# Kernel tuning notes

Measured on AMD Instinct MI355X. Metric: run time of the kernel, lower is better.

## Reference

```python
import jax, jax.numpy as jnp
import numpy as np

EPS = 1e-5      # BatchNorm1d eps
THETA = 1.0     # spike threshold
ALPHA = 5.0     # ATan surrogate alpha

@jax.custom_vjp
def atan_spike(x):
    # forward: heaviside; backward: ATan surrogate gradient
    return (x > 0).astype(x.dtype)

def _spike_fwd(x):
    return atan_spike(x), x

def _spike_bwd(x, g):
    return (g * ALPHA / (2.0 * (1.0 + (jnp.pi / 2.0 * ALPHA * x) ** 2)),)

atan_spike.defvjp(_spike_fwd, _spike_bwd)

def _lif_layer(x, W, beta_raw, gamma, bias, readout):
    # x: [T,B,J], W: [I,J]
    x = jnp.einsum('tbj,ij->tbi', x, W)
    # BatchNorm1d over (T*B) samples, per channel (training-mode batch stats)
    mean = jnp.mean(x, axis=(0, 1))
    var = jnp.var(x, axis=(0, 1))
    x = (x - mean) * jax.lax.rsqrt(var + EPS) * gamma + bias
    beta = jax.nn.sigmoid(beta_raw)
    B, I = x.shape[1], x.shape[2]
    U0 = jnp.zeros((B, I), x.dtype)
    if readout:
        def step(Ut, xt):
            Ut = beta * Ut + (1.0 - beta) * xt
            return Ut, Ut
        _, o = jax.lax.scan(step, U0, x)
    else:
        def step(carry, xt):
            Ut, St = carry
            Ut = beta * (Ut - THETA * St) + (1.0 - beta) * xt
            St = atan_spike(Ut - THETA)
            return (Ut, St), St
        _, o = jax.lax.scan(step, (U0, U0), x)
    return o  # [T,B,I]

def setup_inputs():
    key = jax.random.key(0)
    ks = jax.random.split(key, 8)
    B, T, J, H, O = 128, 512, 700, 512, 20
    def kaiming(k, out_dim, in_dim):
        # kaiming_uniform_(a=sqrt(5)) -> bound = 1/sqrt(fan_in)
        bound = 1.0 / np.sqrt(in_dim)
        return jax.random.uniform(k, (out_dim, in_dim), jnp.float32, -bound, bound)
    return {
        'x': jax.random.normal(ks[0], (B, T, J), jnp.float32),
        'W1': kaiming(ks[1], H, J),
        'beta1': jax.random.uniform(ks[2], (H,), jnp.float32, 0.0, 1.0),
        'g1': jnp.ones((H,), jnp.float32),
        'b1': jnp.zeros((H,), jnp.float32),
        'W2': kaiming(ks[3], H, H),
        'beta2': jax.random.uniform(ks[4], (H,), jnp.float32, 0.0, 1.0),
        'g2': jnp.ones((H,), jnp.float32),
        'b2': jnp.zeros((H,), jnp.float32),
        'Wr': kaiming(ks[5], O, H),
        'betar': jax.random.uniform(ks[6], (O,), jnp.float32, 0.0, 1.0),
        'gr': jnp.ones((O,), jnp.float32),
        'br': jnp.zeros((O,), jnp.float32),
    }

def reference(x, W1, beta1, g1, b1, W2, beta2, g2, b2, Wr, betar, gr, br):
    h = jnp.transpose(x, (1, 0, 2))  # [B,T,J] -> [T,B,J]
    h = _lif_layer(h, W1, beta1, g1, b1, readout=False)
    h = _lif_layer(h, W2, beta2, g2, b2, readout=False)
    h = _lif_layer(h, Wr, betar, gr, br, readout=True)
    p = jax.nn.softmax(h, axis=2)  # [T,B,O]
    return p.sum(axis=0)           # [B,O]
```

## Files before the change

kernel.cpp:

```cpp
#include <hip/hip_runtime.h>
#include <math.h>

typedef _Float16 f16_t;
typedef _Float16 f16x2 __attribute__((ext_vector_type(2)));
typedef _Float16 f16x8 __attribute__((ext_vector_type(8)));
typedef float f32x4 __attribute__((ext_vector_type(4)));

constexpr int Bn = 128;
constexpr int Tn = 512;
constexpr int Jn = 700;
constexpr int Jp = 704;
constexpr int Hn = 512;
constexpr int On = 20;
constexpr int Mn = Bn * Tn;

#define LDS_U32(p) ((__attribute__((address_space(3))) uint32_t*)(p))
#define GLB_U32(p) ((const __attribute__((address_space(1))) uint32_t*)(p))

template <int NT, bool SWZ>
__global__ __launch_bounds__(512, 4) void gemm_f16(
    const f16_t* __restrict__ A, const f16_t* __restrict__ W,
    float* __restrict__ C, float* __restrict__ s_out, float* __restrict__ q_out,
    int LDA, int LDW, int pairs, int Nout)
{
    constexpr int JT = 2 * NT;
    __shared__ __align__(16) f16_t sA[2 * 4096];
    __shared__ __align__(16) f16_t sW[2 * NT * 4096];

    int bx, by;
    if (SWZ) {
        const int g = blockIdx.x;
        by = (g >> 4) * 8 + (g & 7);
        bx = (g >> 3) & 1;
    } else {
        bx = blockIdx.x;
        by = blockIdx.y;
    }
    const int tid  = threadIdx.x;
    const int bm   = by * 128;
    const int bn   = bx * (NT * 128);
    const int lane = tid & 63;
    const int wv   = tid >> 6;
    const int wm   = (wv & 1) * 64;
    const int wn   = (wv >> 1) * (NT * 32);
    const int fr   = lane & 15;
    const int quad = lane >> 4;
    const int srow = lane >> 2;
    const int scol = (((lane & 3) ^ ((lane >> 3) & 3)) * 8);
    const int ksw  = ((quad ^ ((fr >> 1) & 3)) * 8);

    f32x4 acc[4][JT];
#pragma unroll
    for (int i = 0; i < 4; ++i)
#pragma unroll
        for (int j = 0; j < JT; ++j) acc[i][j] = {0.f, 0.f, 0.f, 0.f};

    for (int p = 0; p < pairs; ++p) {
#pragma unroll
        for (int cc = 0; cc < 2; ++cc) {
            const int c  = wv + cc * 8;
            const int s  = c >> 3;
            const int cr = (c & 7) * 16;
            const int kA = p * 64 + s * 32;
            const uint32_t off = __builtin_amdgcn_readfirstlane(s * 8192 + cr * 64);
            const f16_t* gp = A + (size_t)(bm + cr + srow) * LDA + kA + scol;
            __builtin_amdgcn_global_load_lds(GLB_U32(gp), LDS_U32((char*)sA + off), 16, 0, 0);
        }
#pragma unroll
        for (int cc = 0; cc < 2 * NT; ++cc) {
            const int c   = wv + cc * 8;
            const int h   = c / (NT * 8);
            const int rem = c % (NT * 8);
            const int nt  = rem >> 3;
            const int cr  = (rem & 7) * 16;
            const int kW  = p * 64 + h * 32;
            const uint32_t off = __builtin_amdgcn_readfirstlane((h * NT + nt) * 8192 + cr * 64);
            const f16_t* gp = W + (size_t)(bn + nt * 128 + cr + srow) * LDW + kW + scol;
            __builtin_amdgcn_global_load_lds(GLB_U32(gp), LDS_U32((char*)sW + off), 16, 0, 0);
        }
        __syncthreads();

#pragma unroll
        for (int h = 0; h < 2; ++h) {
            f16x8 av[4];
#pragma unroll
            for (int i = 0; i < 4; ++i)
                av[i] = *(const f16x8*)&sA[h * 4096 + (wm + i * 16 + fr) * 32 + ksw];
            f16x8 wf[JT];
#pragma unroll
            for (int jt = 0; jt < JT; ++jt) {
                const int n = wn + jt * 16 + fr;
                wf[jt] = *(const f16x8*)&sW[(h * NT + (n >> 7)) * 4096 + (n & 127) * 32 + ksw];
            }
#pragma unroll
            for (int i = 0; i < 4; ++i)
#pragma unroll
                for (int jt = 0; jt < JT; ++jt)
                    acc[i][jt] = __builtin_amdgcn_mfma_f32_16x16x32_f16(av[i], wf[jt], acc[i][jt], 0, 0, 0);
        }
        __syncthreads();
    }

#pragma unroll
    for (int jt = 0; jt < JT; ++jt) {
        const int gcol = bn + wn + jt * 16 + fr;
        float s = 0.f, q = 0.f;
        if (gcol < Nout) {
#pragma unroll
            for (int i = 0; i < 4; ++i) {
#pragma unroll
                for (int rg = 0; rg < 4; ++rg) {
                    const float v = acc[i][jt][rg];
                    C[(size_t)(bm + wm + i * 16 + quad * 4 + rg) * Nout + gcol] = v;
                    s += v;
                    q += v * v;
                }
            }
        }
        s += __shfl_xor(s, 16); s += __shfl_xor(s, 32);
        q += __shfl_xor(q, 16); q += __shfl_xor(q, 32);
        if (quad == 0 && gcol < Nout) {
            atomicAdd(&s_out[gcol], s);
            atomicAdd(&q_out[gcol], q);
        }
    }
}

__global__ __launch_bounds__(256) void conv_x(const float* __restrict__ x,
                                              f16_t* __restrict__ A1) {
    const int idx = blockIdx.x * 256 + threadIdx.x;
    const int m = idx / 88, g = idx % 88;
    const int k8 = g * 8;
    const float* rp = x + (size_t)m * Jn + k8;
    float f[8];
    if (k8 + 8 <= Jn) {
        const float4 v0 = *(const float4*)rp;
        const float4 v1 = *(const float4*)(rp + 4);
        f[0] = v0.x; f[1] = v0.y; f[2] = v0.z; f[3] = v0.w;
        f[4] = v1.x; f[5] = v1.y; f[6] = v1.z; f[7] = v1.w;
    } else {
#pragma unroll
        for (int e = 0; e < 8; ++e) f[e] = (k8 + e < Jn) ? rp[e] : 0.f;
    }
    f16x8 hv;
#pragma unroll
    for (int e = 0; e < 8; ++e) hv[e] = (f16_t)f[e];
    *(f16x8*)&A1[(size_t)m * Jp + k8] = hv;
}

__global__ __launch_bounds__(256) void conv_w(const float* __restrict__ Wsrc,
                                              f16_t* __restrict__ Wo,
                                              int N, int K, int KP, int NP) {
    const int idx = blockIdx.x * 256 + threadIdx.x;
    if (idx >= NP * (KP / 8)) return;
    const int n = idx / (KP / 8), g = idx % (KP / 8);
    const int k8 = g * 8;
    f16x8 hv;
#pragma unroll
    for (int e = 0; e < 8; ++e) {
        const float f = (n < N && k8 + e < K) ? Wsrc[(size_t)n * K + k8 + e] : 0.f;
        hv[e] = (f16_t)f;
    }
    *(f16x8*)&Wo[(size_t)n * KP + k8] = hv;
}

__global__ __launch_bounds__(256) void lif_scan(const float* __restrict__ X,
                                                f16_t* __restrict__ S_out,
                                                const float* __restrict__ sums,
                                                const float* __restrict__ sumsq,
                                                const float* __restrict__ beta_raw,
                                                const float* __restrict__ gamma,
                                                const float* __restrict__ bias) {
    const int gid = blockIdx.x * 256 + threadIdx.x;
    const int b  = gid >> 8;
    const int cq = gid & 255;
    const int i0 = cq * 2;

    float g[2], bi[2], bt[2], ob[2];
#pragma unroll
    for (int e = 0; e < 2; ++e) {
        const int i = i0 + e;
        const float invM = 1.f / (float)Mn;
        const float mean = sums[i] * invM;
        const float var  = sumsq[i] * invM - mean * mean;
        const float inv  = rsqrtf(var + 1e-5f);
        g[e]  = gamma[i] * inv;
        bi[e] = bias[i] - mean * g[e];
        bt[e] = 1.f / (1.f + expf(-beta_raw[i]));
        ob[e] = 1.f - bt[e];
    }

    const float2* Xp = (const float2*)(X + (size_t)b * Tn * Hn) + cq;
    f16x2* Sp2 = (f16x2*)(S_out + (size_t)b * Tn * Hn) + cq;

    float U[2] = {0.f, 0.f}, Sp[2] = {0.f, 0.f};
#pragma unroll 8
    for (int t = 0; t < Tn; ++t) {
        const float2 v = Xp[(size_t)t * (Hn / 2)];
        const float vf[2] = {v.x, v.y};
        f16x2 so;
#pragma unroll
        for (int e = 0; e < 2; ++e) {
            const float xt = vf[e] * g[e] + bi[e];
            U[e] = bt[e] * (U[e] - Sp[e]) + ob[e] * xt;
            Sp[e] = (U[e] > 1.0f) ? 1.0f : 0.0f;
            so[e] = (f16_t)Sp[e];
        }
        Sp2[(size_t)t * (Hn / 2)] = so;
    }
}

__global__ __launch_bounds__(256) void readout_kernel(const float* __restrict__ A,
                                                      const float* __restrict__ sums,
                                                      const float* __restrict__ sumsq,
                                                      const float* __restrict__ beta_raw,
                                                      const float* __restrict__ gamma,
                                                      const float* __restrict__ bias,
                                                      float* __restrict__ out) {
    __shared__ float xs[Tn * On];
    __shared__ float gsh[On], bsh[On], betash[On];
    __shared__ float red[4][On];

    const int b = blockIdx.x;
    const int tid = threadIdx.x;

    if (tid < On) {
        const float invM = 1.f / (float)Mn;
        const float mean = sums[tid] * invM;
        const float var = sumsq[tid] * invM - mean * mean;
        const float inv = rsqrtf(var + 1e-5f);
        const float g = gamma[tid] * inv;
        gsh[tid] = g;
        bsh[tid] = bias[tid] - mean * g;
        betash[tid] = 1.f / (1.f + expf(-beta_raw[tid]));
    }
    __syncthreads();

    const float* Ab = A + (size_t)b * Tn * On;
    for (int idx = tid; idx < Tn * On; idx += 256) {
        const int o = idx % On;
        xs[idx] = Ab[idx] * gsh[o] + bsh[o];
    }
    __syncthreads();

    if (tid < On) {
        const float beta = betash[tid], omb = 1.f - beta;
        float U = 0.f;
        for (int t = 0; t < Tn; ++t) {
            U = beta * U + omb * xs[t * On + tid];
            xs[t * On + tid] = U;
        }
    }
    __syncthreads();

    float part[On];
#pragma unroll
    for (int o = 0; o < On; ++o) part[o] = 0.f;

    for (int t = tid; t < Tn; t += 256) {
        float v[On];
        float m = -1e30f;
#pragma unroll
        for (int o = 0; o < On; ++o) {
            v[o] = xs[t * On + o];
            m = fmaxf(m, v[o]);
        }
        float s = 0.f;
#pragma unroll
        for (int o = 0; o < On; ++o) {
            v[o] = expf(v[o] - m);
            s += v[o];
        }
        const float rs = 1.f / s;
#pragma unroll
        for (int o = 0; o < On; ++o) part[o] += v[o] * rs;
    }

#pragma unroll
    for (int o = 0; o < On; ++o) {
#pragma unroll
        for (int off = 32; off > 0; off >>= 1) part[o] += __shfl_down(part[o], off);
    }
    const int lane = tid & 63, wid = tid >> 6;
    if (lane == 0) {
#pragma unroll
        for (int o = 0; o < On; ++o) red[wid][o] = part[o];
    }
    __syncthreads();
    if (tid < On) out[b * On + tid] = red[0][tid] + red[1][tid] + red[2][tid] + red[3][tid];
}

extern "C" void kernel_launch(void* const* d_in, const int* in_sizes, int n_in,
                              void* d_out, int out_size, void* d_ws, size_t ws_size,
                              hipStream_t stream) {
    const float* x   = (const float*)d_in[0];
    const float* W1  = (const float*)d_in[1];
    const float* be1 = (const float*)d_in[2];
    const float* g1  = (const float*)d_in[3];
    const float* b1  = (const float*)d_in[4];
    const float* W2  = (const float*)d_in[5];
    const float* be2 = (const float*)d_in[6];
    const float* b2g = (const float*)d_in[7];
    const float* b2  = (const float*)d_in[8];
    const float* Wr  = (const float*)d_in[9];
    const float* ber = (const float*)d_in[10];
    const float* gr  = (const float*)d_in[11];
    const float* br  = (const float*)d_in[12];
    float* out = (float*)d_out;

    char* ws = (char*)d_ws;
    const size_t r0Bytes   = (size_t)Mn * Jp * sizeof(f16_t);
    const size_t bufCBytes = (size_t)Mn * Hn * sizeof(float);
    f16_t* A1   = (f16_t*)ws;
    f16_t* bufS = (f16_t*)ws;
    float* bufC = (float*)(ws + r0Bytes);
    char*  p    = ws + r0Bytes + bufCBytes;
    float* bufR = (float*)p;              p += (size_t)Mn * On * sizeof(float);
    f16_t* W1h  = (f16_t*)p;              p += (size_t)Hn * Jp * sizeof(f16_t);
    f16_t* W2h  = (f16_t*)p;              p += (size_t)Hn * Hn * sizeof(f16_t);
    f16_t* Wrh  = (f16_t*)p;              p += (size_t)128 * Hn * sizeof(f16_t);
    float* stats = (float*)p;
    float* s1 = stats;       float* q1 = s1 + Hn;
    float* s2 = q1 + Hn;     float* q2 = s2 + Hn;
    float* s3 = q2 + Hn;     float* q3 = s3 + 32;

    hipMemsetAsync(stats, 0, (4 * Hn + 64) * sizeof(float), stream);

    conv_x<<<(Mn * 88) / 256, 256, 0, stream>>>(x, A1);
    conv_w<<<(Hn * 88 + 255) / 256, 256, 0, stream>>>(W1, W1h, Hn, Jn, Jp, Hn);
    conv_w<<<(Hn * 64 + 255) / 256, 256, 0, stream>>>(W2, W2h, Hn, Hn, Hn, Hn);
    conv_w<<<(128 * 64 + 255) / 256, 256, 0, stream>>>(Wr, Wrh, On, Hn, Hn, 128);

    gemm_f16<2, true><<<2 * (Mn / 128), 512, 0, stream>>>(A1, W1h, bufC, s1, q1,
        Jp, Jp, Jp / 64, Hn);
    lif_scan<<<(Bn * Hn / 2) / 256, 256, 0, stream>>>(bufC, bufS, s1, q1, be1, g1, b1);

    gemm_f16<2, true><<<2 * (Mn / 128), 512, 0, stream>>>(bufS, W2h, bufC, s2, q2,
        Hn, Hn, Hn / 64, Hn);
    lif_scan<<<(Bn * Hn / 2) / 256, 256, 0, stream>>>(bufC, bufS, s2, q2, be2, b2g, b2);

    gemm_f16<1, false><<<dim3(1, Mn / 128), 512, 0, stream>>>(bufS, Wrh, bufR, s3, q3,
        Hn, Hn, Hn / 64, On);
    readout_kernel<<<Bn, 256, 0, stream>>>(bufR, s3, q3, ber, gr, br, out);
}
```

Before: 561.8 us.

## Double-buffer LDS tiles in f16 GEMM to overlap global loads with MFMA

Doubles the LDS staging buffers for the A and W tiles and prefetches the next K-pair into the alternate buffer while the current one is consumed by MFMAs. Explicit vmcnt waits and raw barriers replace __syncthreads. Launch-bound minimum occupancy is now a template parameter, lowered to 2 for the large GEMMs. The extra LDS footprint lowers the possible number of resident workgroups per CU, trading occupancy for latency hiding.

```diff
diff --git a/kernel.cpp b/kernel.cpp
--- a/kernel.cpp
+++ b/kernel.cpp
@@ -17,15 +17,15 @@
 #define LDS_U32(p) ((__attribute__((address_space(3))) uint32_t*)(p))
 #define GLB_U32(p) ((const __attribute__((address_space(1))) uint32_t*)(p))
 
-template <int NT, bool SWZ>
-__global__ __launch_bounds__(512, 4) void gemm_f16(
+template <int NT, bool SWZ, int MINW>
+__global__ __launch_bounds__(512, MINW) void gemm_f16(
     const f16_t* __restrict__ A, const f16_t* __restrict__ W,
     float* __restrict__ C, float* __restrict__ s_out, float* __restrict__ q_out,
     int LDA, int LDW, int pairs, int Nout)
 {
     constexpr int JT = 2 * NT;
-    __shared__ __align__(16) f16_t sA[2 * 4096];
-    __shared__ __align__(16) f16_t sW[2 * NT * 4096];
+    __shared__ __align__(16) f16_t sA[2 * 2 * 4096];
+    __shared__ __align__(16) f16_t sW[2 * 2 * NT * 4096];
 
     int bx, by;
     if (SWZ) {
@@ -55,14 +55,15 @@
 #pragma unroll
         for (int j = 0; j < JT; ++j) acc[i][j] = {0.f, 0.f, 0.f, 0.f};
 
-    for (int p = 0; p < pairs; ++p) {
+    auto stage = [&](int buf, int p) {
 #pragma unroll
         for (int cc = 0; cc < 2; ++cc) {
             const int c  = wv + cc * 8;
             const int s  = c >> 3;
             const int cr = (c & 7) * 16;
             const int kA = p * 64 + s * 32;
-            const uint32_t off = __builtin_amdgcn_readfirstlane(s * 8192 + cr * 64);
+            const uint32_t off =
+                __builtin_amdgcn_readfirstlane(buf * 16384 + s * 8192 + cr * 64);
             const f16_t* gp = A + (size_t)(bm + cr + srow) * LDA + kA + scol;
             __builtin_amdgcn_global_load_lds(GLB_U32(gp), LDS_U32((char*)sA + off), 16, 0, 0);
         }
@@ -74,23 +75,38 @@
             const int nt  = rem >> 3;
             const int cr  = (rem & 7) * 16;
             const int kW  = p * 64 + h * 32;
-            const uint32_t off = __builtin_amdgcn_readfirstlane((h * NT + nt) * 8192 + cr * 64);
+            const uint32_t off = __builtin_amdgcn_readfirstlane(
+                buf * (NT * 16384) + (h * NT + nt) * 8192 + cr * 64);
             const f16_t* gp = W + (size_t)(bn + nt * 128 + cr + srow) * LDW + kW + scol;
             __builtin_amdgcn_global_load_lds(GLB_U32(gp), LDS_U32((char*)sW + off), 16, 0, 0);
         }
-        __syncthreads();
-
+    };
+
+    stage(0, 0);
+    int cur = 0;
+    for (int p = 0; p < pairs; ++p) {
+        if (p + 1 < pairs) {
+            stage(cur ^ 1, p + 1);
+            asm volatile("s_waitcnt vmcnt(%0)" :: "i"(2 + 2 * NT) : "memory");
+        } else {
+            asm volatile("s_waitcnt vmcnt(0)" ::: "memory");
+        }
+        __builtin_amdgcn_s_barrier();
+        __builtin_amdgcn_sched_barrier(0);
+
+        const int aBase = cur * 8192;
+        const int wBase = cur * (NT * 8192);
 #pragma unroll
         for (int h = 0; h < 2; ++h) {
             f16x8 av[4];
 #pragma unroll
             for (int i = 0; i < 4; ++i)
-                av[i] = *(const f16x8*)&sA[h * 4096 + (wm + i * 16 + fr) * 32 + ksw];
+                av[i] = *(const f16x8*)&sA[aBase + h * 4096 + (wm + i * 16 + fr) * 32 + ksw];
             f16x8 wf[JT];
 #pragma unroll
             for (int jt = 0; jt < JT; ++jt) {
                 const int n = wn + jt * 16 + fr;
-                wf[jt] = *(const f16x8*)&sW[(h * NT + (n >> 7)) * 4096 + (n & 127) * 32 + ksw];
+                wf[jt] = *(const f16x8*)&sW[wBase + (h * NT + (n >> 7)) * 4096 + (n & 127) * 32 + ksw];
             }
 #pragma unroll
             for (int i = 0; i < 4; ++i)
@@ -98,7 +114,11 @@
                 for (int jt = 0; jt < JT; ++jt)
                     acc[i][jt] = __builtin_amdgcn_mfma_f32_16x16x32_f16(av[i], wf[jt], acc[i][jt], 0, 0, 0);
         }
-        __syncthreads();
+
+        asm volatile("s_waitcnt lgkmcnt(0)" ::: "memory");
+        __builtin_amdgcn_s_barrier();
+        __builtin_amdgcn_sched_barrier(0);
+        cur ^= 1;
     }
 
 #pragma unroll
@@ -331,15 +351,15 @@
     conv_w<<<(Hn * 64 + 255) / 256, 256, 0, stream>>>(W2, W2h, Hn, Hn, Hn, Hn);
     conv_w<<<(128 * 64 + 255) / 256, 256, 0, stream>>>(Wr, Wrh, On, Hn, Hn, 128);
 
-    gemm_f16<2, true><<<2 * (Mn / 128), 512, 0, stream>>>(A1, W1h, bufC, s1, q1,
+    gemm_f16<2, true, 2><<<2 * (Mn / 128), 512, 0, stream>>>(A1, W1h, bufC, s1, q1,
         Jp, Jp, Jp / 64, Hn);
     lif_scan<<<(Bn * Hn / 2) / 256, 256, 0, stream>>>(bufC, bufS, s1, q1, be1, g1, b1);
 
-    gemm_f16<2, true><<<2 * (Mn / 128), 512, 0, stream>>>(bufS, W2h, bufC, s2, q2,
+    gemm_f16<2, true, 2><<<2 * (Mn / 128), 512, 0, stream>>>(bufS, W2h, bufC, s2, q2,
         Hn, Hn, Hn / 64, Hn);
     lif_scan<<<(Bn * Hn / 2) / 256, 256, 0, stream>>>(bufC, bufS, s2, q2, be2, b2g, b2);
 
-    gemm_f16<1, false><<<dim3(1, Mn / 128), 512, 0, stream>>>(bufS, Wrh, bufR, s3, q3,
+    gemm_f16<1, false, 4><<<dim3(1, Mn / 128), 512, 0, stream>>>(bufS, Wrh, bufR, s3, q3,
         Hn, Hn, Hn / 64, On);
     readout_kernel<<<Bn, 256, 0, stream>>>(bufR, s3, q3, ber, gr, br, out);
 }
```

Result: slower. 593.4 us (+5.6%).

## Fuse fp32-to-fp16 input conversion into first GEMM's A-tile load

Applied to the files above, without the earlier changes.

Removes the separate conv_x kernel, which read the fp32 input and wrote a padded fp16 copy. The first GEMM now loads fp32 x directly into registers, converts it to fp16 and stores it into the swizzled LDS tile, with zero padding at the K tail. This drops a full write and re-read of the large fp16 activation buffer and one kernel launch. In exchange, the A path uses synchronous register loads instead of asynchronous global-to-LDS loads, and fp32 reads are repeated across the two column-block workgroups.

```diff
diff --git a/kernel.cpp b/kernel.cpp
--- a/kernel.cpp
+++ b/kernel.cpp
@@ -17,9 +17,10 @@
 #define LDS_U32(p) ((__attribute__((address_space(3))) uint32_t*)(p))
 #define GLB_U32(p) ((const __attribute__((address_space(1))) uint32_t*)(p))
 
-template <int NT, bool SWZ>
+template <int NT, bool SWZ, bool FUSEA>
 __global__ __launch_bounds__(512, 4) void gemm_f16(
-    const f16_t* __restrict__ A, const f16_t* __restrict__ W,
+    const f16_t* __restrict__ A, const float* __restrict__ Xf,
+    const f16_t* __restrict__ W,
     float* __restrict__ C, float* __restrict__ s_out, float* __restrict__ q_out,
     int LDA, int LDW, int pairs, int Nout)
 {
@@ -49,6 +50,10 @@
     const int scol = (((lane & 3) ^ ((lane >> 3) & 3)) * 8);
     const int ksw  = ((quad ^ ((fr >> 1) & 3)) * 8);
 
+    const int fs  = tid >> 8;
+    const int frw = (tid >> 1) & 127;
+    const int fh  = tid & 1;
+
     f32x4 acc[4][JT];
 #pragma unroll
     for (int i = 0; i < 4; ++i)
@@ -56,15 +61,33 @@
         for (int j = 0; j < JT; ++j) acc[i][j] = {0.f, 0.f, 0.f, 0.f};
 
     for (int p = 0; p < pairs; ++p) {
-#pragma unroll
-        for (int cc = 0; cc < 2; ++cc) {
-            const int c  = wv + cc * 8;
-            const int s  = c >> 3;
-            const int cr = (c & 7) * 16;
-            const int kA = p * 64 + s * 32;
-            const uint32_t off = __builtin_amdgcn_readfirstlane(s * 8192 + cr * 64);
-            const f16_t* gp = A + (size_t)(bm + cr + srow) * LDA + kA + scol;
-            __builtin_amdgcn_global_load_lds(GLB_U32(gp), LDS_U32((char*)sA + off), 16, 0, 0);
+        float fbuf[16];
+        if constexpr (FUSEA) {
+            const int col0 = p * 64 + fs * 32 + fh * 16;
+            const float* xp = Xf + (size_t)(bm + frw) * LDA + col0;
+            if (col0 + 16 <= LDA) {
+#pragma unroll
+                for (int q4 = 0; q4 < 4; ++q4) {
+                    const float4 v = *(const float4*)(xp + q4 * 4);
+                    fbuf[q4 * 4 + 0] = v.x; fbuf[q4 * 4 + 1] = v.y;
+                    fbuf[q4 * 4 + 2] = v.z; fbuf[q4 * 4 + 3] = v.w;
+                }
+            } else {
+#pragma unroll
+                for (int e = 0; e < 16; ++e)
+                    fbuf[e] = (col0 + e < LDA) ? xp[e] : 0.f;
+            }
+        } else {
+#pragma unroll
+            for (int cc = 0; cc < 2; ++cc) {
+                const int c  = wv + cc * 8;
+                const int s  = c >> 3;
+                const int cr = (c & 7) * 16;
+                const int kA = p * 64 + s * 32;
+                const uint32_t off = __builtin_amdgcn_readfirstlane(s * 8192 + cr * 64);
+                const f16_t* gp = A + (size_t)(bm + cr + srow) * LDA + kA + scol;
+                __builtin_amdgcn_global_load_lds(GLB_U32(gp), LDS_U32((char*)sA + off), 16, 0, 0);
+            }
         }
 #pragma unroll
         for (int cc = 0; cc < 2 * NT; ++cc) {
@@ -78,6 +101,17 @@
             const f16_t* gp = W + (size_t)(bn + nt * 128 + cr + srow) * LDW + kW + scol;
             __builtin_amdgcn_global_load_lds(GLB_U32(gp), LDS_U32((char*)sW + off), 16, 0, 0);
         }
+        if constexpr (FUSEA) {
+            const int m = (frw >> 1) & 3;
+#pragma unroll
+            for (int c = 0; c < 2; ++c) {
+                f16x8 hv;
+#pragma unroll
+                for (int e = 0; e < 8; ++e) hv[e] = (f16_t)fbuf[c * 8 + e];
+                const int lc = (fh * 2 + c) ^ m;
+                *(f16x8*)((char*)sA + fs * 8192 + frw * 64 + lc * 16) = hv;
+            }
+        }
         __syncthreads();
 
 #pragma unroll
@@ -124,28 +158,6 @@
             atomicAdd(&q_out[gcol], q);
         }
     }
-}
-
-__global__ __launch_bounds__(256) void conv_x(const float* __restrict__ x,
-                                              f16_t* __restrict__ A1) {
-    const int idx = blockIdx.x * 256 + threadIdx.x;
-    const int m = idx / 88, g = idx % 88;
-    const int k8 = g * 8;
-    const float* rp = x + (size_t)m * Jn + k8;
-    float f[8];
-    if (k8 + 8 <= Jn) {
-        const float4 v0 = *(const float4*)rp;
-        const float4 v1 = *(const float4*)(rp + 4);
-        f[0] = v0.x; f[1] = v0.y; f[2] = v0.z; f[3] = v0.w;
-        f[4] = v1.x; f[5] = v1.y; f[6] = v1.z; f[7] = v1.w;
-    } else {
-#pragma unroll
-        for (int e = 0; e < 8; ++e) f[e] = (k8 + e < Jn) ? rp[e] : 0.f;
-    }
-    f16x8 hv;
-#pragma unroll
-    for (int e = 0; e < 8; ++e) hv[e] = (f16_t)f[e];
-    *(f16x8*)&A1[(size_t)m * Jp + k8] = hv;
 }
 
 __global__ __launch_bounds__(256) void conv_w(const float* __restrict__ Wsrc,
@@ -311,7 +323,6 @@
     char* ws = (char*)d_ws;
     const size_t r0Bytes   = (size_t)Mn * Jp * sizeof(f16_t);
     const size_t bufCBytes = (size_t)Mn * Hn * sizeof(float);
-    f16_t* A1   = (f16_t*)ws;
     f16_t* bufS = (f16_t*)ws;
     float* bufC = (float*)(ws + r0Bytes);
     char*  p    = ws + r0Bytes + bufCBytes;
@@ -326,20 +337,19 @@
 
     hipMemsetAsync(stats, 0, (4 * Hn + 64) * sizeof(float), stream);
 
-    conv_x<<<(Mn * 88) / 256, 256, 0, stream>>>(x, A1);
     conv_w<<<(Hn * 88 + 255) / 256, 256, 0, stream>>>(W1, W1h, Hn, Jn, Jp, Hn);
     conv_w<<<(Hn * 64 + 255) / 256, 256, 0, stream>>>(W2, W2h, Hn, Hn, Hn, Hn);
     conv_w<<<(128 * 64 + 255) / 256, 256, 0, stream>>>(Wr, Wrh, On, Hn, Hn, 128);
 
-    gemm_f16<2, true><<<2 * (Mn / 128), 512, 0, stream>>>(A1, W1h, bufC, s1, q1,
-        Jp, Jp, Jp / 64, Hn);
+    gemm_f16<2, true, true><<<2 * (Mn / 128), 512, 0, stream>>>(nullptr, x, W1h,
+        bufC, s1, q1, Jn, Jp, Jp / 64, Hn);
     lif_scan<<<(Bn * Hn / 2) / 256, 256, 0, stream>>>(bufC, bufS, s1, q1, be1, g1, b1);
 
-    gemm_f16<2, true><<<2 * (Mn / 128), 512, 0, stream>>>(bufS, W2h, bufC, s2, q2,
-        Hn, Hn, Hn / 64, Hn);
+    gemm_f16<2, true, false><<<2 * (Mn / 128), 512, 0, stream>>>(bufS, nullptr, W2h,
+        bufC, s2, q2, Hn, Hn, Hn / 64, Hn);
     lif_scan<<<(Bn * Hn / 2) / 256, 256, 0, stream>>>(bufC, bufS, s2, q2, be2, b2g, b2);
 
-    gemm_f16<1, false><<<dim3(1, Mn / 128), 512, 0, stream>>>(bufS, Wrh, bufR, s3, q3,
-        Hn, Hn, Hn / 64, On);
+    gemm_f16<1, false, false><<<dim3(1, Mn / 128), 512, 0, stream>>>(bufS, nullptr, Wrh,
+        bufR, s3, q3, Hn, Hn, Hn / 64, On);
     readout_kernel<<<Bn, 256, 0, stream>>>(bufR, s3, q3, ber, gr, br, out);
 }
```

Measured after the change: 601.9 us. 7.1% more time.
